# Performance work log

Measured on AMD Instinct MI355X. Metric: run time of the kernel, lower is better.

## Reference

```python
import jax, jax.numpy as jnp
import numpy as np

N_NODES = 100000
N_EDGES = 1000000
D_FEAT = 64


def setup_inputs() -> dict:
    key = jax.random.key(0)
    k1, k2, k3, k4 = jax.random.split(key, 4)
    feat = jax.random.normal(k1, (N_NODES, D_FEAT), dtype=jnp.float32)
    edge_weight = jax.random.uniform(k2, (N_EDGES,), dtype=jnp.float32)
    edge_src = jax.random.randint(k3, (N_EDGES,), 0, N_NODES, dtype=jnp.int64)
    edge_dst = jax.random.randint(k4, (N_EDGES,), 0, N_NODES, dtype=jnp.int64)
    return {"feat": feat, "edge_weight": edge_weight,
            "edge_src": edge_src, "edge_dst": edge_dst}


def reference(feat, edge_weight, edge_src, edge_dst):
    # Original module reverses edges: graph((edges()[1], edges()[0])), then
    # u_mul_e('h','_edge_weight') + sum. So in terms of the ORIGINAL edge
    # orientation (edge_src -> edge_dst):
    #   out[edge_src] += feat[edge_dst] * edge_weight
    msgs = feat[edge_dst] * edge_weight[:, None]          # [E, D] gather + scale
    out = jax.ops.segment_sum(msgs, edge_src, num_segments=feat.shape[0])
    return out
```

## Files before the change

### kernel.cpp

```cpp
#include <hip/hip_runtime.h>


#define D_FEAT    64
#define SB        512
#define SB_SHIFT  9
#define CAPB      6144
#define BIN_CHUNK 4096
#define BIN_THR   512
#define CONV_BLK  128

__device__ __forceinline__ ushort f2bf(float f) {
    unsigned u = __float_as_uint(f);
    unsigned r = (u + 0x7fff + ((u >> 16) & 1)) >> 16;
    return (ushort)r;
}
__device__ __forceinline__ float bf_lo(unsigned u) { return __uint_as_float(u << 16); }
__device__ __forceinline__ float bf_hi(unsigned u) { return __uint_as_float(u & 0xffff0000u); }

__global__ __launch_bounds__(BIN_THR) void bin_conv(
    const float* __restrict__ feat, ushort* __restrict__ fh, int total4,
    const int* __restrict__ src, const int* __restrict__ dst,
    const float* __restrict__ w, int* __restrict__ cursor,
    int2* __restrict__ ep, int E, int NB, int nbin)
{
    if ((int)blockIdx.x >= nbin) {
        int cb = blockIdx.x - nbin;
        for (int i = cb * BIN_THR + threadIdx.x; i < total4; i += CONV_BLK * BIN_THR) {
            float4 v = reinterpret_cast<const float4*>(feat)[i];
            ushort4 o;
            o.x = f2bf(v.x); o.y = f2bf(v.y); o.z = f2bf(v.z); o.w = f2bf(v.w);
            reinterpret_cast<ushort4*>(fh)[i] = o;
        }
        return;
    }
    extern __shared__ int sh[];
    int* cnt   = sh;
    int* basel = sh + NB;
    for (int b = threadIdx.x; b < NB; b += BIN_THR) cnt[b] = 0;
    __syncthreads();
    int start = blockIdx.x * BIN_CHUNK;
    int end   = min(start + BIN_CHUNK, E);
    for (int e = start + threadIdx.x; e < end; e += BIN_THR)
        atomicAdd(&cnt[src[e] >> SB_SHIFT], 1);
    __syncthreads();
    for (int b = threadIdx.x; b < NB; b += BIN_THR) {
        int c = cnt[b];
        basel[b] = c ? atomicAdd(&cursor[b], c) : 0;
    }
    __syncthreads();
    for (int b = threadIdx.x; b < NB; b += BIN_THR) cnt[b] = 0;
    __syncthreads();
    for (int e = start + threadIdx.x; e < end; e += BIN_THR) {
        int s  = src[e];
        int b  = s >> SB_SHIFT;
        int ls = s & (SB - 1);
        int r  = atomicAdd(&cnt[b], 1);
        ep[(size_t)b * CAPB + basel[b] + r] =
            make_int2(dst[e] | (ls << 17), __float_as_int(w[e]));
    }
}

__global__ __launch_bounds__(512) void node_sort(
    const int* __restrict__ cursor, int2* __restrict__ ep,
    int* __restrict__ node_off, int* __restrict__ node_end, int N)
{
    __shared__ int2 eb[CAPB];
    __shared__ int cnt[SB];
    __shared__ int cur[SB];
    __shared__ int sh[SB];
    int b = blockIdx.x, t = threadIdx.x;
    cnt[t] = 0;
    __syncthreads();
    int sz = min(cursor[b], CAPB);
    int base = b * CAPB;
    for (int i = t; i < sz; i += 512) {
        int2 e = ep[base + i];
        eb[i] = e;
        atomicAdd(&cnt[(e.x >> 17) & (SB - 1)], 1);
    }
    __syncthreads();
    int c = cnt[t];
    sh[t] = c;
    __syncthreads();
    for (int off = 1; off < 512; off <<= 1) {
        int x = (t >= off) ? sh[t - off] : 0;
        __syncthreads();
        sh[t] += x;
        __syncthreads();
    }
    int excl = sh[t] - c;
    cur[t] = excl;
    int node = b * SB + t;
    if (node < N) {
        node_off[node] = base + excl;
        node_end[node] = base + excl + c;
    }
    __syncthreads();
    for (int i = t; i < sz; i += 512) {
        int2 e  = eb[i];
        int ls  = (e.x >> 17) & (SB - 1);
        int pos = atomicAdd(&cur[ls], 1);
        ep[base + pos] = make_int2(e.x & 0x1FFFF, e.y);
    }
}

__global__ __launch_bounds__(256) void segment_bf16(
    const ushort* __restrict__ fh, const int* __restrict__ node_off,
    const int* __restrict__ node_end, const int2* __restrict__ ep,
    float* __restrict__ out, int N)
{
    int tid  = blockIdx.x * blockDim.x + threadIdx.x;
    int node = tid >> 3;
    int q    = tid & 7;
    if (node >= N) return;
    int j   = node_off[node];
    int end = node_end[node];
    float a0 = 0.f, a1 = 0.f, a2 = 0.f, a3 = 0.f;
    float a4 = 0.f, a5 = 0.f, a6 = 0.f, a7 = 0.f;
    for (; j + 4 <= end; j += 4) {
        int2 e0 = ep[j],     e1 = ep[j + 1];
        int2 e2 = ep[j + 2], e3 = ep[j + 3];
        uint4 h0 = *reinterpret_cast<const uint4*>(&fh[(size_t)e0.x * D_FEAT + q * 8]);
        uint4 h1 = *reinterpret_cast<const uint4*>(&fh[(size_t)e1.x * D_FEAT + q * 8]);
        uint4 h2 = *reinterpret_cast<const uint4*>(&fh[(size_t)e2.x * D_FEAT + q * 8]);
        uint4 h3 = *reinterpret_cast<const uint4*>(&fh[(size_t)e3.x * D_FEAT + q * 8]);
        float w0 = __int_as_float(e0.y), w1 = __int_as_float(e1.y);
        float w2 = __int_as_float(e2.y), w3 = __int_as_float(e3.y);
        a0 += bf_lo(h0.x) * w0; a1 += bf_hi(h0.x) * w0;
        a2 += bf_lo(h0.y) * w0; a3 += bf_hi(h0.y) * w0;
        a4 += bf_lo(h0.z) * w0; a5 += bf_hi(h0.z) * w0;
        a6 += bf_lo(h0.w) * w0; a7 += bf_hi(h0.w) * w0;
        a0 += bf_lo(h1.x) * w1; a1 += bf_hi(h1.x) * w1;
        a2 += bf_lo(h1.y) * w1; a3 += bf_hi(h1.y) * w1;
        a4 += bf_lo(h1.z) * w1; a5 += bf_hi(h1.z) * w1;
        a6 += bf_lo(h1.w) * w1; a7 += bf_hi(h1.w) * w1;
        a0 += bf_lo(h2.x) * w2; a1 += bf_hi(h2.x) * w2;
        a2 += bf_lo(h2.y) * w2; a3 += bf_hi(h2.y) * w2;
        a4 += bf_lo(h2.z) * w2; a5 += bf_hi(h2.z) * w2;
        a6 += bf_lo(h2.w) * w2; a7 += bf_hi(h2.w) * w2;
        a0 += bf_lo(h3.x) * w3; a1 += bf_hi(h3.x) * w3;
        a2 += bf_lo(h3.y) * w3; a3 += bf_hi(h3.y) * w3;
        a4 += bf_lo(h3.z) * w3; a5 += bf_hi(h3.z) * w3;
        a6 += bf_lo(h3.w) * w3; a7 += bf_hi(h3.w) * w3;
    }
    for (; j < end; j++) {
        int2 e = ep[j];
        uint4 h = *reinterpret_cast<const uint4*>(&fh[(size_t)e.x * D_FEAT + q * 8]);
        float ww = __int_as_float(e.y);
        a0 += bf_lo(h.x) * ww; a1 += bf_hi(h.x) * ww;
        a2 += bf_lo(h.y) * ww; a3 += bf_hi(h.y) * ww;
        a4 += bf_lo(h.z) * ww; a5 += bf_hi(h.z) * ww;
        a6 += bf_lo(h.w) * ww; a7 += bf_hi(h.w) * ww;
    }
    float* o = &out[(size_t)node * D_FEAT + q * 8];
    *reinterpret_cast<float4*>(o)     = float4{a0, a1, a2, a3};
    *reinterpret_cast<float4*>(o + 4) = float4{a4, a5, a6, a7};
}

extern "C" void kernel_launch(void* const* d_in, const int* in_sizes, int n_in,
                              void* d_out, int out_size, void* d_ws, size_t ws_size,
                              hipStream_t stream) {
    const float* feat = (const float*)d_in[0];
    const float* w    = (const float*)d_in[1];
    const int*   src  = (const int*)d_in[2];
    const int*   dst  = (const int*)d_in[3];
    float* out = (float*)d_out;

    int N  = out_size / D_FEAT;
    int E  = in_sizes[1];
    int NB = (N + SB - 1) / SB;

    int* cursor   = (int*)d_ws;
    int* node_off = cursor + NB;
    int* node_end = node_off + N;
    uintptr_t ap = ((uintptr_t)(node_end + N) + 15) & ~(uintptr_t)15;
    int2* ep = (int2*)ap;
    ushort* fh = (ushort*)(ep + (size_t)NB * CAPB);

    hipMemsetAsync(cursor, 0, (size_t)NB * sizeof(int), stream);

    int nbin = (E + BIN_CHUNK - 1) / BIN_CHUNK;
    size_t lds_bin = 2 * (size_t)NB * sizeof(int);
    int total4 = N * D_FEAT / 4;

    bin_conv<<<nbin + CONV_BLK, BIN_THR, lds_bin, stream>>>(
        feat, fh, total4, src, dst, w, cursor, ep, E, NB, nbin);
    node_sort<<<NB, 512, 0, stream>>>(cursor, ep, node_off, node_end, N);

    long long segthreads = (long long)N * 8;
    segment_bf16<<<(int)((segthreads + 255) / 256), 256, 0, stream>>>(
        fh, node_off, node_end, ep, out, N);
}
```

Baseline: 73.93 us.

## Slice feature dims across blocks, stage src in LDS, wave-shuffle scan

Result: slower. 93.29 us (+26.2%).

```diff
diff --git a/kernel.cpp b/kernel.cpp
--- a/kernel.cpp
+++ b/kernel.cpp
@@ -8,6 +8,7 @@
 #define BIN_CHUNK 4096
 #define BIN_THR   512
 #define CONV_BLK  128
+#define CH        64
 
 __device__ __forceinline__ ushort f2bf(float f) {
     unsigned u = __float_as_uint(f);
@@ -36,12 +37,16 @@
     extern __shared__ int sh[];
     int* cnt   = sh;
     int* basel = sh + NB;
+    int* stage = sh + 2 * NB;
     for (int b = threadIdx.x; b < NB; b += BIN_THR) cnt[b] = 0;
     __syncthreads();
     int start = blockIdx.x * BIN_CHUNK;
     int end   = min(start + BIN_CHUNK, E);
-    for (int e = start + threadIdx.x; e < end; e += BIN_THR)
-        atomicAdd(&cnt[src[e] >> SB_SHIFT], 1);
+    for (int e = start + threadIdx.x; e < end; e += BIN_THR) {
+        int s = src[e];
+        stage[e - start] = s;
+        atomicAdd(&cnt[s >> SB_SHIFT], 1);
+    }
     __syncthreads();
     for (int b = threadIdx.x; b < NB; b += BIN_THR) {
         int c = cnt[b];
@@ -51,7 +56,7 @@
     for (int b = threadIdx.x; b < NB; b += BIN_THR) cnt[b] = 0;
     __syncthreads();
     for (int e = start + threadIdx.x; e < end; e += BIN_THR) {
-        int s  = src[e];
+        int s  = stage[e - start];
         int b  = s >> SB_SHIFT;
         int ls = s & (SB - 1);
         int r  = atomicAdd(&cnt[b], 1);
@@ -67,7 +72,7 @@
     __shared__ int2 eb[CAPB];
     __shared__ int cnt[SB];
     __shared__ int cur[SB];
-    __shared__ int sh[SB];
+    __shared__ int wpre[8];
     int b = blockIdx.x, t = threadIdx.x;
     cnt[t] = 0;
     __syncthreads();
@@ -80,15 +85,22 @@
     }
     __syncthreads();
     int c = cnt[t];
-    sh[t] = c;
-    __syncthreads();
-    for (int off = 1; off < 512; off <<= 1) {
-        int x = (t >= off) ? sh[t - off] : 0;
-        __syncthreads();
-        sh[t] += x;
-        __syncthreads();
-    }
-    int excl = sh[t] - c;
+    int lane = t & 63, wv = t >> 6;
+    int x = c;
+    #pragma unroll
+    for (int d = 1; d < 64; d <<= 1) {
+        int y = __shfl_up(x, d, 64);
+        if (lane >= d) x += y;
+    }
+    if (lane == 63) wpre[wv] = x;
+    __syncthreads();
+    if (t == 0) {
+        int run = 0;
+        #pragma unroll
+        for (int k = 0; k < 8; k++) { int v = wpre[k]; wpre[k] = run; run += v; }
+    }
+    __syncthreads();
+    int excl = x - c + wpre[wv];
     cur[t] = excl;
     int node = b * SB + t;
     if (node < N) {
@@ -104,15 +116,20 @@
     }
 }
 
-__global__ __launch_bounds__(256) void segment_bf16(
+__global__ __launch_bounds__(256) void segment_sliced(
     const ushort* __restrict__ fh, const int* __restrict__ node_off,
     const int* __restrict__ node_end, const int2* __restrict__ ep,
-    float* __restrict__ out, int N)
+    float* __restrict__ out, int N, int NCH)
 {
-    int tid  = blockIdx.x * blockDim.x + threadIdx.x;
-    int node = tid >> 3;
-    int q    = tid & 7;
+    int g = blockIdx.x & 7;
+    int i = blockIdx.x >> 3;
+    int slice = g & 1;
+    int c = i * 4 + (g >> 1);
+    if (c >= NCH) return;
+    int node = c * CH + (threadIdx.x >> 2);
+    int q4   = threadIdx.x & 3;
     if (node >= N) return;
+    int foff = slice * 32 + q4 * 8;
     int j   = node_off[node];
     int end = node_end[node];
     float a0 = 0.f, a1 = 0.f, a2 = 0.f, a3 = 0.f;
@@ -120,10 +137,10 @@
     for (; j + 4 <= end; j += 4) {
         int2 e0 = ep[j],     e1 = ep[j + 1];
         int2 e2 = ep[j + 2], e3 = ep[j + 3];
-        uint4 h0 = *reinterpret_cast<const uint4*>(&fh[(size_t)e0.x * D_FEAT + q * 8]);
-        uint4 h1 = *reinterpret_cast<const uint4*>(&fh[(size_t)e1.x * D_FEAT + q * 8]);
-        uint4 h2 = *reinterpret_cast<const uint4*>(&fh[(size_t)e2.x * D_FEAT + q * 8]);
-        uint4 h3 = *reinterpret_cast<const uint4*>(&fh[(size_t)e3.x * D_FEAT + q * 8]);
+        uint4 h0 = *reinterpret_cast<const uint4*>(&fh[(size_t)e0.x * D_FEAT + foff]);
+        uint4 h1 = *reinterpret_cast<const uint4*>(&fh[(size_t)e1.x * D_FEAT + foff]);
+        uint4 h2 = *reinterpret_cast<const uint4*>(&fh[(size_t)e2.x * D_FEAT + foff]);
+        uint4 h3 = *reinterpret_cast<const uint4*>(&fh[(size_t)e3.x * D_FEAT + foff]);
         float w0 = __int_as_float(e0.y), w1 = __int_as_float(e1.y);
         float w2 = __int_as_float(e2.y), w3 = __int_as_float(e3.y);
         a0 += bf_lo(h0.x) * w0; a1 += bf_hi(h0.x) * w0;
@@ -145,14 +162,14 @@
     }
     for (; j < end; j++) {
         int2 e = ep[j];
-        uint4 h = *reinterpret_cast<const uint4*>(&fh[(size_t)e.x * D_FEAT + q * 8]);
+        uint4 h = *reinterpret_cast<const uint4*>(&fh[(size_t)e.x * D_FEAT + foff]);
         float ww = __int_as_float(e.y);
         a0 += bf_lo(h.x) * ww; a1 += bf_hi(h.x) * ww;
         a2 += bf_lo(h.y) * ww; a3 += bf_hi(h.y) * ww;
         a4 += bf_lo(h.z) * ww; a5 += bf_hi(h.z) * ww;
         a6 += bf_lo(h.w) * ww; a7 += bf_hi(h.w) * ww;
     }
-    float* o = &out[(size_t)node * D_FEAT + q * 8];
+    float* o = &out[(size_t)node * D_FEAT + foff];
     *reinterpret_cast<float4*>(o)     = float4{a0, a1, a2, a3};
     *reinterpret_cast<float4*>(o + 4) = float4{a4, a5, a6, a7};
 }
@@ -180,14 +197,15 @@
     hipMemsetAsync(cursor, 0, (size_t)NB * sizeof(int), stream);
 
     int nbin = (E + BIN_CHUNK - 1) / BIN_CHUNK;
-    size_t lds_bin = 2 * (size_t)NB * sizeof(int);
+    size_t lds_bin = (2 * (size_t)NB + BIN_CHUNK) * sizeof(int);
     int total4 = N * D_FEAT / 4;
 
     bin_conv<<<nbin + CONV_BLK, BIN_THR, lds_bin, stream>>>(
         feat, fh, total4, src, dst, w, cursor, ep, E, NB, nbin);
     node_sort<<<NB, 512, 0, stream>>>(cursor, ep, node_off, node_end, N);
 
-    long long segthreads = (long long)N * 8;
-    segment_bf16<<<(int)((segthreads + 255) / 256), 256, 0, stream>>>(
-        fh, node_off, node_end, ep, out, N);
-}
+    int NCH = (N + CH - 1) / CH;
+    int segblocks = 8 * ((NCH + 3) / 4);
+    segment_sliced<<<segblocks, 256, 0, stream>>>(
+        fh, node_off, node_end, ep, out, N, NCH);
+}
```
